# Performance work log

Hardware: AMD Instinct MI355X
Metric: run time of the kernel (lower is better)

The kernel has to match this reference:

```python
import jax, jax.numpy as jnp
import numpy as np

B, N = 2, 8192

PARAM_SHAPES = {
    'down0_w': (32, 3), 'down0_b': (32,),
    'sc1_w1': (32, 35), 'sc1_b1': (32,), 'sc1_w2': (64, 32), 'sc1_b2': (64,),
    'sc2_w1': (64, 67), 'sc2_b1': (64,), 'sc2_w2': (128, 64), 'sc2_b2': (128,),
    'sc3_w1': (128, 131), 'sc3_b1': (128,), 'sc3_w2': (192, 128), 'sc3_b2': (192,),
    'sc4_w1': (192, 195), 'sc4_b1': (192,), 'sc4_w2': (192, 192), 'sc4_b2': (192,),
    'up4_w1': (192, 195), 'up4_b1': (192,), 'up4_w2': (192, 384), 'up4_b2': (192,),
    'up3_w1': (128, 195), 'up3_b1': (128,), 'up3_w2': (128, 256), 'up3_b2': (128,),
    'up2_w1': (64, 131), 'up2_b1': (64,), 'up2_w2': (64, 128), 'up2_b2': (64,),
    'up1_w1': (32, 67), 'up1_b1': (32,), 'up1_w2': (32, 64), 'up1_b2': (32,),
}
PNAMES = list(PARAM_SHAPES.keys())


def _fps(xyz, m):
    # xyz [N,3] -> [m] int32 farthest-point-sample indices (deterministic, start at point 0)
    def body(dmin, _):
        nxt = jnp.argmax(dmin)
        d = jnp.sum((xyz - xyz[nxt]) ** 2, -1)
        return jnp.minimum(dmin, d), nxt.astype(jnp.int32)
    d0 = jnp.sum((xyz - xyz[0]) ** 2, -1)
    _, rest = jax.lax.scan(body, d0, None, length=m - 1)
    return jnp.concatenate([jnp.zeros((1,), jnp.int32), rest])


def _gather(pts, idx):
    # pts [B,N,C], idx [B,...] -> [B,...,C]
    return jax.vmap(lambda p, i: p[i])(pts, idx)


def _ball_query(new_xyz, xyz, radius, k):
    # first-k points within radius, invalid slots filled with the first valid index
    d2 = jnp.sum((new_xyz[:, :, None, :] - xyz[:, None, :, :]) ** 2, -1)  # [B,M,N]
    n = xyz.shape[1]
    order = jnp.where(d2 <= radius * radius, jnp.arange(n)[None, None, :], n)
    idx = jnp.argsort(order, axis=-1)[..., :k]
    valid = jnp.take_along_axis(order, idx, -1) < n
    return jnp.where(valid, idx, idx[..., :1])


def _knn(query, ref, k):
    d2 = jnp.sum((query[:, :, None, :] - ref[:, None, :, :]) ** 2, -1)  # [B,Nq,Nr]
    _, idx = jax.lax.top_k(-d2, k)
    return idx


def _mlp(h, w, b):
    # pointwise shared MLP layer with ReLU on channel-last tensor
    return jax.nn.relu(jnp.einsum('...c,oc->...o', h, w) + b)


def _set_conv(xyz, feat, npoint, radius, k, w1, b1, w2, b2):
    # PointNet++-style SetConv: FPS -> ball-query group -> shared MLP -> max-pool
    fps_idx = jax.vmap(_fps, (0, None))(xyz, npoint)          # [B,M]
    new_xyz = _gather(xyz, fps_idx)                            # [B,M,3]
    gi = _ball_query(new_xyz, xyz, radius, k)                  # [B,M,k]
    h = jnp.concatenate([_gather(xyz, gi) - new_xyz[:, :, None, :], _gather(feat, gi)], -1)
    h = _mlp(_mlp(h, w1, b1), w2, b2)                          # [B,M,k,Cout]
    return new_xyz, fps_idx, jnp.max(h, axis=2)


def _set_upconv(s_xyz, d_xyz, s_feat, d_feat, k, w1, b1, w2, b2):
    # FlowNet3D-style SetUpConv: kNN from dense to sparse -> MLP -> max-pool -> fuse with dense feat
    gi = _knn(d_xyz, s_xyz, k)                                 # [B,Nd,k]
    h = jnp.concatenate([_gather(s_xyz, gi) - d_xyz[:, :, None, :], _gather(s_feat, gi)], -1)
    pooled = jnp.max(_mlp(h, w1, b1), axis=2)                  # [B,Nd,m1]
    return _mlp(jnp.concatenate([pooled, d_feat], -1), w2, b2)


def _encoder(pc, feat, p):
    xyz = jnp.transpose(pc, (0, 2, 1))                         # [B,N,3]
    f0 = _mlp(jnp.transpose(feat, (0, 2, 1)), p['down0_w'], p['down0_b'])  # [B,N,32]
    xyz1, i1, f1 = _set_conv(xyz, f0, 2048, 0.5, 16, p['sc1_w1'], p['sc1_b1'], p['sc1_w2'], p['sc1_b2'])
    xyz2, i2, f2 = _set_conv(xyz1, f1, 512, 1.0, 16, p['sc2_w1'], p['sc2_b1'], p['sc2_w2'], p['sc2_b2'])
    xyz3, i3, f3 = _set_conv(xyz2, f2, 128, 2.0, 16, p['sc3_w1'], p['sc3_b1'], p['sc3_w2'], p['sc3_b2'])
    xyz4, i4, f4 = _set_conv(xyz3, f3, 64, 4.0, 16, p['sc4_w1'], p['sc4_b1'], p['sc4_w2'], p['sc4_b2'])
    u3 = _set_upconv(xyz4, xyz3, f4, f3, 8, p['up4_w1'], p['up4_b1'], p['up4_w2'], p['up4_b2'])
    u2 = _set_upconv(xyz3, xyz2, u3, f2, 8, p['up3_w1'], p['up3_b1'], p['up3_w2'], p['up3_b2'])
    u1 = _set_upconv(xyz2, xyz1, u2, f1, 8, p['up2_w1'], p['up2_b1'], p['up2_w2'], p['up2_b2'])
    u0 = _set_upconv(xyz1, xyz, u1, f0, 8, p['up1_w1'], p['up1_b1'], p['up1_w2'], p['up1_b2'])
    return (xyz1, xyz2, xyz3), (i1, i2, i3), (u0, u1, u2, u3)


def setup_inputs() -> dict:
    key = jax.random.key(0)
    ks = jax.random.split(key, 2 + len(PNAMES))
    inp = {
        'pc': jax.random.normal(ks[0], (B, 3, N), jnp.float32),
        'feat': jax.random.normal(ks[1], (B, 3, N), jnp.float32),
    }
    for i, name in enumerate(PNAMES):
        inp[name] = jax.random.normal(ks[2 + i], PARAM_SHAPES[name], jnp.float32) * 0.05
    return inp


def reference(pc, feat, down0_w, down0_b, sc1_w1, sc1_b1, sc1_w2, sc1_b2, sc2_w1, sc2_b1, sc2_w2, sc2_b2, sc3_w1, sc3_b1, sc3_w2, sc3_b2, sc4_w1, sc4_b1, sc4_w2, sc4_b2, up4_w1, up4_b1, up4_w2, up4_b2, up3_w1, up3_b1, up3_w2, up3_b2, up2_w1, up2_b1, up2_w2, up2_b2, up1_w1, up1_b1, up1_w2, up1_b2):
    # GenFlow_unit.forward with gts[0] is None -> pure encoder path
    loc = locals()
    p = {k: loc[k] for k in PNAMES}
    (x1, x2, x3), (i1, i2, i3), (u0, u1, u2, u3) = _encoder(pc, feat, p)
    t = lambda a: jnp.transpose(a, (0, 2, 1))  # back to torch channel-first convention
    return (t(x1), t(x2), t(x3), i1, i2, i3, t(u0), t(u1), t(u2), t(u3))
```

## Files before the change

### kernel.cpp

```cpp
#include <hip/hip_runtime.h>
#include <hip/hip_bf16.h>
#include <cstdint>

#define DEV __device__ __forceinline__

typedef float f32x2 __attribute__((ext_vector_type(2)));

DEV float sqdist(float ax, float ay, float az, float bx, float by, float bz) {
    float dx = __fsub_rn(ax, bx), dy = __fsub_rn(ay, by), dz = __fsub_rn(az, bz);
    return __fadd_rn(__fadd_rn(__fmul_rn(dx, dx), __fmul_rn(dy, dy)), __fmul_rn(dz, dz));
}

DEV f32x2 sqdist2(f32x2 ax, f32x2 ay, f32x2 az, float bx, float by, float bz) {
#pragma clang fp contract(off)
    f32x2 dx = ax - bx, dy = ay - by, dz = az - bz;
    return (dx * dx + dy * dy) + dz * dz;
}

DEV unsigned short f2bf(float f) {
    unsigned int u = __float_as_uint(f);
    u += 0x7fffu + ((u >> 16) & 1u);
    return (unsigned short)(u >> 16);
}

DEV float bf2f(unsigned short u) { return __uint_as_float(((unsigned int)u) << 16); }

template <int CTRL>
DEV int dpp_i(int v) { return __builtin_amdgcn_update_dpp(v, v, CTRL, 0xf, 0xf, false); }
template <int CTRL>
DEV float dpp_f(float v) { return __int_as_float(dpp_i<CTRL>(__float_as_int(v))); }

enum : int {
    O_X1 = 0, O_X2 = 12288, O_X3 = 15360,
    O_I1 = 16128, O_I2 = 20224, O_I3 = 21248,
    O_U0 = 21504, O_U1 = 545792, O_U2 = 807936, O_U3 = 939008
};

__global__ __launch_bounds__(256) void k_init(const float* __restrict__ pc,
                                              const float* __restrict__ feat,
                                              const float* __restrict__ w0,
                                              const float* __restrict__ b0,
                                              float* __restrict__ xyz,
                                              unsigned short* __restrict__ f0) {
    const int N = 8192;
    int i = blockIdx.x * blockDim.x + threadIdx.x;
    if (i >= 2 * N) return;
    int b = i / N, n = i % N;
    float fx0 = feat[(b * 3 + 0) * N + n];
    float fx1 = feat[(b * 3 + 1) * N + n];
    float fx2 = feat[(b * 3 + 2) * N + n];
    xyz[i * 3 + 0] = pc[(b * 3 + 0) * N + n];
    xyz[i * 3 + 1] = pc[(b * 3 + 1) * N + n];
    xyz[i * 3 + 2] = pc[(b * 3 + 2) * N + n];
#pragma unroll
    for (int o = 0; o < 32; o++) {
        float acc = b0[o];
        acc = fmaf(w0[o * 3 + 0], fx0, acc);
        acc = fmaf(w0[o * 3 + 1], fx1, acc);
        acc = fmaf(w0[o * 3 + 2], fx2, acc);
        f0[(size_t)i * 32 + o] = f2bf(fmaxf(acc, 0.f));
    }
}

template <int N, int T>
__global__ __launch_bounds__(T) void k_bin(const float* __restrict__ xyz,
                                           float* __restrict__ xp, float* __restrict__ yp,
                                           float* __restrict__ zp, int* __restrict__ pid) {
    constexpr int W = T / 64;
    int b = blockIdx.x, t = threadIdx.x;
    const float* X = xyz + (size_t)b * N * 3;
    __shared__ float smn[3][W], smx[3][W];
    __shared__ int hist[512], scan[512], cnt[512];
    float mn[3] = {3e38f, 3e38f, 3e38f}, mx[3] = {-3e38f, -3e38f, -3e38f};
    for (int p = t; p < N; p += T) {
        float v[3] = {X[p * 3], X[p * 3 + 1], X[p * 3 + 2]};
#pragma unroll
        for (int a = 0; a < 3; a++) { mn[a] = fminf(mn[a], v[a]); mx[a] = fmaxf(mx[a], v[a]); }
    }
#pragma unroll
    for (int a = 0; a < 3; a++) {
#pragma unroll
        for (int m = 1; m < 64; m <<= 1) {
            mn[a] = fminf(mn[a], __shfl_xor(mn[a], m, 64));
            mx[a] = fmaxf(mx[a], __shfl_xor(mx[a], m, 64));
        }
    }
    if ((t & 63) == 0) {
#pragma unroll
        for (int a = 0; a < 3; a++) { smn[a][t >> 6] = mn[a]; smx[a][t >> 6] = mx[a]; }
    }
    for (int i = t; i < 512; i += T) { hist[i] = 0; cnt[i] = 0; }
    __syncthreads();
#pragma unroll
    for (int a = 0; a < 3; a++) {
        mn[a] = smn[a][0]; mx[a] = smx[a][0];
#pragma unroll
        for (int w = 1; w < W; w++) { mn[a] = fminf(mn[a], smn[a][w]); mx[a] = fmaxf(mx[a], smx[a][w]); }
    }
    float inv[3];
#pragma unroll
    for (int a = 0; a < 3; a++) inv[a] = 8.0f / fmaxf(mx[a] - mn[a], 1e-9f);
    auto bin_of = [&](float x, float y, float z) {
        int ix = min(7, max(0, (int)((x - mn[0]) * inv[0])));
        int iy = min(7, max(0, (int)((y - mn[1]) * inv[1])));
        int iz = min(7, max(0, (int)((z - mn[2]) * inv[2])));
        return (ix << 6) | (iy << 3) | iz;
    };
    for (int p = t; p < N; p += T) {
        atomicAdd(&hist[bin_of(X[p * 3], X[p * 3 + 1], X[p * 3 + 2])], 1);
    }
    __syncthreads();
    if (t < 512) scan[t] = hist[t];
    __syncthreads();
    for (int s = 1; s < 512; s <<= 1) {
        int v = 0;
        if (t < 512 && t >= s) v = scan[t - s];
        __syncthreads();
        if (t < 512) scan[t] += v;
        __syncthreads();
    }
    for (int p = t; p < N; p += T) {
        float x = X[p * 3], y = X[p * 3 + 1], z = X[p * 3 + 2];
        int bid = bin_of(x, y, z);
        int pos = (scan[bid] - hist[bid]) + atomicAdd(&cnt[bid], 1);
        xp[(size_t)b * N + pos] = x;
        yp[(size_t)b * N + pos] = y;
        zp[(size_t)b * N + pos] = z;
        pid[(size_t)b * N + pos] = p;
    }
}

template <int N, int M, int T>
__global__ __launch_bounds__(T, 1) void k_fps_pruned(
    const float* __restrict__ xp, const float* __restrict__ yp,
    const float* __restrict__ zp, const int* __restrict__ pidg,
    const float* __restrict__ xyz, int* __restrict__ idx_out) {
    constexpr int P = N / T;
    constexpr int P2 = P / 2;
    int b = blockIdx.x, t = threadIdx.x;
    const float* XP = xp + (size_t)b * N;
    const float* YP = yp + (size_t)b * N;
    const float* ZP = zp + (size_t)b * N;
    const int* PIDG = pidg + (size_t)b * N;
    __shared__ float sx[N], sy[N], sz[N];
    __shared__ int spid[N];
    __shared__ unsigned long long skey[3];
    f32x2 px[P2], py[P2], pz[P2], dmin[P2];
    float c0x = xyz[(size_t)b * N * 3 + 0];
    float c0y = xyz[(size_t)b * N * 3 + 1];
    float c0z = xyz[(size_t)b * N * 3 + 2];
    int base = t * P;
    float blx = 3e38f, bly = 3e38f, blz = 3e38f, bhx = -3e38f, bhy = -3e38f, bhz = -3e38f;
#pragma unroll
    for (int i = 0; i < P2; i++) {
        int p0 = base + 2 * i, p1 = p0 + 1;
        px[i] = f32x2{XP[p0], XP[p1]};
        py[i] = f32x2{YP[p0], YP[p1]};
        pz[i] = f32x2{ZP[p0], ZP[p1]};
        sx[p0] = px[i].x; sy[p0] = py[i].x; sz[p0] = pz[i].x;
        sx[p1] = px[i].y; sy[p1] = py[i].y; sz[p1] = pz[i].y;
        spid[p0] = PIDG[p0]; spid[p1] = PIDG[p1];
        blx = fminf(blx, fminf(px[i].x, px[i].y)); bhx = fmaxf(bhx, fmaxf(px[i].x, px[i].y));
        bly = fminf(bly, fminf(py[i].x, py[i].y)); bhy = fmaxf(bhy, fmaxf(py[i].x, py[i].y));
        blz = fminf(blz, fminf(pz[i].x, pz[i].y)); bhz = fmaxf(bhz, fmaxf(pz[i].x, pz[i].y));
        dmin[i] = sqdist2(px[i], py[i], pz[i], c0x, c0y, c0z);
    }
    if (t == 0) {
        idx_out[b * M] = 0;
        skey[0] = 0; skey[1] = 0; skey[2] = 0;
    }
    float bv;
    int bi;
    auto local_argmax = [&]() {
        f32x2 m2[P2];
#pragma unroll
        for (int i = 0; i < P2; i++) m2[i] = dmin[i];
#pragma unroll
        for (int s = P2 / 2; s >= 1; s >>= 1)
#pragma unroll
            for (int i = 0; i < s; i++) m2[i] = __builtin_elementwise_max(m2[i], m2[i + s]);
        bv = fmaxf(m2[0].x, m2[0].y);
        int ii[P];
#pragma unroll
        for (int i = 0; i < P; i++)
            ii[i] = (dmin[i >> 1][i & 1] == bv) ? (base + i) : 0x7fffffff;
#pragma unroll
        for (int s = P / 2; s >= 1; s >>= 1)
#pragma unroll
            for (int i = 0; i < s; i++) ii[i] = min(ii[i], ii[i + s]);
        bi = ii[0];
    };
    float bvw;
    int biw;
    auto wave_reduce = [&]() {
        float bw = bv;
        bw = fmaxf(bw, dpp_f<0x121>(bw));
        bw = fmaxf(bw, dpp_f<0x122>(bw));
        bw = fmaxf(bw, dpp_f<0x124>(bw));
        bw = fmaxf(bw, dpp_f<0x128>(bw));
        bw = fmaxf(bw, dpp_f<0x142>(bw));
        bw = fmaxf(bw, dpp_f<0x143>(bw));
        bvw = __int_as_float(__builtin_amdgcn_readlane(__float_as_int(bw), 63));
        unsigned int im = (bv == bvw) ? (unsigned int)bi : 0xffffffffu;
        im = min(im, (unsigned int)dpp_i<0x121>((int)im));
        im = min(im, (unsigned int)dpp_i<0x122>((int)im));
        im = min(im, (unsigned int)dpp_i<0x124>((int)im));
        im = min(im, (unsigned int)dpp_i<0x128>((int)im));
        im = min(im, (unsigned int)dpp_i<0x142>((int)im));
        im = min(im, (unsigned int)dpp_i<0x143>((int)im));
        biw = __builtin_amdgcn_readlane((int)im, 63);
    };
    local_argmax();
    wave_reduce();
    __syncthreads();
    int jm = 1;
    for (int j = 1; j < M; j++) {
        unsigned long long key =
            ((unsigned long long)__float_as_uint(bvw) << 32) | (unsigned int)~biw;
        if ((t & 63) == 0) atomicMax(&skey[jm], key);
        __syncthreads();
        unsigned long long gk = skey[jm];
        int gi = (int)~(unsigned int)gk;
        if (t == 0) {
            idx_out[b * M + j] = spid[gi];
            skey[jm == 0 ? 2 : jm - 1] = 0;
        }
        jm = (jm == 2) ? 0 : jm + 1;
        float cx = sx[gi], cy = sy[gi], cz = sz[gi];
        float qx = fminf(fmaxf(cx, blx), bhx);
        float qy = fminf(fmaxf(cy, bly), bhy);
        float qz = fminf(fmaxf(cz, blz), bhz);
        float dxb = cx - qx, dyb = cy - qy, dzb = cz - qz;
        float db = dxb * dxb + dyb * dyb + dzb * dzb;
        bool upd = !(db * 0.999f > bv);
        if (upd) {
#pragma unroll
            for (int i = 0; i < P2; i++)
                dmin[i] = __builtin_elementwise_min(
                    dmin[i], sqdist2(px[i], py[i], pz[i], cx, cy, cz));
            local_argmax();
        }
        if (__ballot(upd)) wave_reduce();
    }
}

template <int N, int M, int T>
DEV void fps_body(int b, int t, const float* __restrict__ xyz,
                  int* __restrict__ idx_out, char* smem) {
    constexpr int P = N / T;
    constexpr int P2 = P / 2;
    constexpr int W = T / 64;
    const float* X = xyz + (size_t)b * N * 3;
    float* sx = (float*)smem;
    float* sy = sx + N;
    float* sz = sy + N;
    unsigned long long* skey = (unsigned long long*)(smem + 12 * N);
    f32x2 px[P2], py[P2], pz[P2], dmin[P2];
    float c0x = X[0], c0y = X[1], c0z = X[2];
#pragma unroll
    for (int i = 0; i < P2; i++) {
        int p0 = (2 * i) * T + t, p1 = (2 * i + 1) * T + t;
        px[i] = f32x2{X[p0 * 3 + 0], X[p1 * 3 + 0]};
        py[i] = f32x2{X[p0 * 3 + 1], X[p1 * 3 + 1]};
        pz[i] = f32x2{X[p0 * 3 + 2], X[p1 * 3 + 2]};
        sx[p0] = px[i].x; sy[p0] = py[i].x; sz[p0] = pz[i].x;
        sx[p1] = px[i].y; sy[p1] = py[i].y; sz[p1] = pz[i].y;
        dmin[i] = sqdist2(px[i], py[i], pz[i], c0x, c0y, c0z);
    }
    if (t == 0) {
        idx_out[b * M] = 0;
        skey[0] = 0; skey[1] = 0; skey[2] = 0;
    }
    __syncthreads();
    int jm = 1;
    for (int j = 1; j < M; j++) {
        f32x2 m2[P2];
#pragma unroll
        for (int i = 0; i < P2; i++) m2[i] = dmin[i];
#pragma unroll
        for (int s = P2 / 2; s >= 1; s >>= 1)
#pragma unroll
            for (int i = 0; i < s; i++) m2[i] = __builtin_elementwise_max(m2[i], m2[i + s]);
        float bv = fmaxf(m2[0].x, m2[0].y);
        int ii[P];
#pragma unroll
        for (int i = 0; i < P; i++)
            ii[i] = (dmin[i >> 1][i & 1] == bv) ? (i * T + t) : 0x7fffffff;
#pragma unroll
        for (int s = P / 2; s >= 1; s >>= 1)
#pragma unroll
            for (int i = 0; i < s; i++) ii[i] = min(ii[i], ii[i + s]);
        int bi = ii[0];
        float bw = bv;
        bw = fmaxf(bw, dpp_f<0x121>(bw));
        bw = fmaxf(bw, dpp_f<0x122>(bw));
        bw = fmaxf(bw, dpp_f<0x124>(bw));
        bw = fmaxf(bw, dpp_f<0x128>(bw));
        bw = fmaxf(bw, dpp_f<0x142>(bw));
        bw = fmaxf(bw, dpp_f<0x143>(bw));
        float bvw = __int_as_float(__builtin_amdgcn_readlane(__float_as_int(bw), 63));
        unsigned int im = (bv == bvw) ? (unsigned int)bi : 0xffffffffu;
        im = min(im, (unsigned int)dpp_i<0x121>((int)im));
        im = min(im, (unsigned int)dpp_i<0x122>((int)im));
        im = min(im, (unsigned int)dpp_i<0x124>((int)im));
        im = min(im, (unsigned int)dpp_i<0x128>((int)im));
        im = min(im, (unsigned int)dpp_i<0x142>((int)im));
        im = min(im, (unsigned int)dpp_i<0x143>((int)im));
        int biw = __builtin_amdgcn_readlane((int)im, 63);
        int gi;
        if constexpr (W > 1) {
            unsigned long long key =
                ((unsigned long long)__float_as_uint(bvw) << 32) | (unsigned int)~biw;
            if ((t & 63) == 0) atomicMax(&skey[jm], key);
            __syncthreads();
            unsigned long long gk = skey[jm];
            gi = (int)~(unsigned int)gk;
            if (t == 0) skey[jm == 0 ? 2 : jm - 1] = 0;
            jm = (jm == 2) ? 0 : jm + 1;
        } else {
            gi = biw;
        }
        if (t == 0) idx_out[b * M + j] = gi;
        float cx = sx[gi], cy = sy[gi], cz = sz[gi];
#pragma unroll
        for (int i = 0; i < P2; i++)
            dmin[i] = __builtin_elementwise_min(
                dmin[i], sqdist2(px[i], py[i], pz[i], cx, cy, cz));
    }
}

template <int N, int M, int T>
__global__ __launch_bounds__(T, 1) void k_fps(const float* __restrict__ xyz,
                                              int* __restrict__ idx_out) {
    __shared__ __align__(16) char smem[12 * N + 24];
    fps_body<N, M, T>(blockIdx.x, threadIdx.x, xyz, idx_out, smem);
}

__global__ __launch_bounds__(256) void k_gather(const float* __restrict__ xyz_src,
                                                const int* __restrict__ idx,
                                                float* __restrict__ xyz_dst,
                                                int NS, int M) {
    int i = blockIdx.x * blockDim.x + threadIdx.x;
    if (i >= 2 * M) return;
    int b = i / M;
    int id = idx[i] & (NS - 1);
    xyz_dst[i * 3 + 0] = xyz_src[((size_t)b * NS + id) * 3 + 0];
    xyz_dst[i * 3 + 1] = xyz_src[((size_t)b * NS + id) * 3 + 1];
    xyz_dst[i * 3 + 2] = xyz_src[((size_t)b * NS + id) * 3 + 2];
}

template <int NS, int CF, int CMID, int COUT>
DEV void setconv_body(int q, int bb, int tid, int bdim,
                      const float* __restrict__ X, const unsigned short* __restrict__ F,
                      const float* __restrict__ C, const float* __restrict__ w1,
                      const float* __restrict__ b1, const float* __restrict__ w2,
                      const float* __restrict__ b2, unsigned short* __restrict__ fout,
                      float r2, int M, char* smem) {
    constexpr int CIN = 3 + CF;
    constexpr int K = 16;
    constexpr int M8 = CMID / 8;
    constexpr int O8 = COUT / 8;
    constexpr int MSTR = CMID + 1;
    int blk = bb * M + q;
    const float* Xb = X + (size_t)bb * NS * 3;
    const unsigned short* Fb = F + (size_t)bb * NS * CF;
    int* s_n = (int*)smem;
    int* s_cntp = (int*)(smem + 64);
    float* s_h = (float*)(smem + 80);
    float* s_mid = s_h + K * CIN;
    float* s_pool = s_mid + K * MSTR;
    float cx = C[(size_t)blk * 3 + 0], cy = C[(size_t)blk * 3 + 1], cz = C[(size_t)blk * 3 + 2];
    if (tid < 64) {
        int lane = tid;
        int cnt = 0;
        for (int base = 0; base < NS; base += 64) {
            int p = base + lane;
            float d2 = sqdist(Xb[p * 3], Xb[p * 3 + 1], Xb[p * 3 + 2], cx, cy, cz);
            bool in = (d2 <= r2);
            unsigned long long msk = __ballot(in);
            if (in) {
                int pos = cnt + __popcll(msk & ((1ull << lane) - 1ull));
                if (pos < K) s_n[pos] = p;
            }
            cnt += __popcll(msk);
            if (cnt >= K) break;
        }
        if (lane == 0) *s_cntp = cnt < K ? cnt : K;
    }
    __syncthreads();
    int cnt = *s_cntp;
    if (tid >= cnt && tid < K) s_n[tid] = s_n[0];
    __syncthreads();
    for (int tIdx = tid; tIdx < K * CIN; tIdx += bdim) {
        int n = tIdx / CIN, c = tIdx % CIN;
        int gi = s_n[n];
        float v;
        if (c < 3) v = __fsub_rn(Xb[gi * 3 + c], (c == 0 ? cx : (c == 1 ? cy : cz)));
        else v = bf2f(Fb[(size_t)gi * CF + (c - 3)]);
        s_h[n * CIN + c] = v;
    }
    __syncthreads();
    if (tid < 128) {
        int n = tid >> 3, sub = tid & 7;
#pragma unroll
        for (int j = 0; j < M8; j++) {
            int m = sub * M8 + j;
            float acc = b1[m];
#pragma unroll 4
            for (int c = 0; c < CIN; c++) acc = fmaf(w1[m * CIN + c], s_h[n * CIN + c], acc);
            s_mid[n * MSTR + m] = fmaxf(acc, 0.f);
        }
    }
    __syncthreads();
    if (tid < 128) {
        int n = tid >> 3, sub = tid & 7;
        float vals[O8];
#pragma unroll
        for (int j = 0; j < O8; j++) {
            int o = sub * O8 + j;
            float acc = b2[o];
#pragma unroll 4
            for (int c = 0; c < CMID; c++) acc = fmaf(w2[o * CMID + c], s_mid[n * MSTR + c], acc);
            vals[j] = fmaxf(acc, 0.f);
        }
#pragma unroll
        for (int j = 0; j < O8; j++) {
            vals[j] = fmaxf(vals[j], __shfl_xor(vals[j], 8, 64));
            vals[j] = fmaxf(vals[j], __shfl_xor(vals[j], 16, 64));
            vals[j] = fmaxf(vals[j], __shfl_xor(vals[j], 32, 64));
        }
        int lw = tid & 63, wv = tid >> 6;
        if (lw < 8) {
#pragma unroll
            for (int j = 0; j < O8; j++) s_pool[wv * COUT + lw * O8 + j] = vals[j];
        }
    }
    __syncthreads();
    if (tid < 8) {
#pragma unroll
        for (int j = 0; j < O8; j++) {
            int o = tid * O8 + j;
            fout[(size_t)blk * COUT + o] = f2bf(fmaxf(s_pool[o], s_pool[COUT + o]));
        }
    }
}

template <int NS, int CF, int CMID, int COUT>
__global__ __launch_bounds__(128) void k_setconv(
    const float* __restrict__ X, const unsigned short* __restrict__ F,
    const float* __restrict__ C, const float* __restrict__ w1,
    const float* __restrict__ b1, const float* __restrict__ w2,
    const float* __restrict__ b2, unsigned short* __restrict__ fout,
    float r2, int M) {
    constexpr int K = 16;
    constexpr int CIN = 3 + CF;
    __shared__ __align__(16) char smem[80 + 4 * (K * CIN + K * (CMID + 1) + 2 * COUT)];
    setconv_body<NS, CF, CMID, COUT>(blockIdx.x, blockIdx.y, threadIdx.x, blockDim.x,
                                     X, F, C, w1, b1, w2, b2, fout, r2, M, smem);
}

template <int N, int M, int T, int NS, int CF, int CMID, int COUT>
__global__ __launch_bounds__(T, 1) void k_fps_sc(
    const float* __restrict__ fxyz, int* __restrict__ idx_out,
    const float* __restrict__ X, const unsigned short* __restrict__ F,
    const float* __restrict__ C, const float* __restrict__ w1,
    const float* __restrict__ b1, const float* __restrict__ w2,
    const float* __restrict__ b2, unsigned short* __restrict__ fout,
    float r2, int Msc) {
    constexpr int K = 16;
    constexpr int CIN = 3 + CF;
    constexpr int FPS_B = 12 * N + 24;
    constexpr int SC_B = 80 + 4 * (K * CIN + K * (CMID + 1) + 2 * COUT);
    constexpr int SB = FPS_B > SC_B ? FPS_B : SC_B;
    __shared__ __align__(16) char smem[SB];
    if (blockIdx.x < 2) {
        fps_body<N, M, T>(blockIdx.x, threadIdx.x, fxyz, idx_out, smem);
    } else {
        int lin = blockIdx.x - 2;
        int q = lin % Msc, bb = lin / Msc;
        setconv_body<NS, CF, CMID, COUT>(q, bb, threadIdx.x, blockDim.x,
                                         X, F, C, w1, b1, w2, b2, fout, r2, Msc, smem);
    }
}

template <int S, int CS, int CMID, int CD, int COUT, bool TRANS>
__global__ __launch_bounds__(64) void k_upconv(
    const float* __restrict__ SX, const float* __restrict__ DX,
    const void* __restrict__ SFv, const unsigned short* __restrict__ DF,
    const float* __restrict__ w1, const float* __restrict__ b1,
    const float* __restrict__ w2, const float* __restrict__ b2,
    float* __restrict__ out, int o_off, int ND) {
    constexpr int K = 8;
    constexpr int CIN = 3 + CS;
    constexpr int CIN2 = CMID + CD;
    constexpr int M8 = CMID / 8;
    int q = blockIdx.x, b = blockIdx.y;
    int blk = b * ND + q;
    int lane = threadIdx.x;
    const float* SXb = SX + (size_t)b * S * 3;
    float qx = DX[(size_t)blk * 3], qy = DX[(size_t)blk * 3 + 1], qz = DX[(size_t)blk * 3 + 2];
    __shared__ int s_k[K];
    __shared__ float s_h[K][CIN];
    __shared__ float s_in2[CIN2];
    float bd[K];
    int bi[K];
#pragma unroll
    for (int i = 0; i < K; i++) { bd[i] = 3.0e38f; bi[i] = 0x7fffffff; }
    for (int p = lane; p < S; p += 64) {
        float d2 = sqdist(SXb[p * 3], SXb[p * 3 + 1], SXb[p * 3 + 2], qx, qy, qz);
        if (d2 < bd[K - 1] || (d2 == bd[K - 1] && p < bi[K - 1])) {
            bd[K - 1] = d2; bi[K - 1] = p;
#pragma unroll
            for (int j = K - 1; j > 0; j--) {
                bool sw = (bd[j] < bd[j - 1]) || (bd[j] == bd[j - 1] && bi[j] < bi[j - 1]);
                if (sw) {
                    float tv = bd[j]; bd[j] = bd[j - 1]; bd[j - 1] = tv;
                    int ti = bi[j]; bi[j] = bi[j - 1]; bi[j - 1] = ti;
                }
            }
        }
    }
    for (int r = 0; r < K; r++) {
        float vv = bd[0];
        float bw = vv;
        bw = fminf(bw, dpp_f<0x121>(bw));
        bw = fminf(bw, dpp_f<0x122>(bw));
        bw = fminf(bw, dpp_f<0x124>(bw));
        bw = fminf(bw, dpp_f<0x128>(bw));
        bw = fminf(bw, dpp_f<0x142>(bw));
        bw = fminf(bw, dpp_f<0x143>(bw));
        float vw = __int_as_float(__builtin_amdgcn_readlane(__float_as_int(bw), 63));
        unsigned int im = (vv == vw) ? (unsigned int)bi[0] : 0xffffffffu;
        im = min(im, (unsigned int)dpp_i<0x121>((int)im));
        im = min(im, (unsigned int)dpp_i<0x122>((int)im));
        im = min(im, (unsigned int)dpp_i<0x124>((int)im));
        im = min(im, (unsigned int)dpp_i<0x128>((int)im));
        im = min(im, (unsigned int)dpp_i<0x142>((int)im));
        im = min(im, (unsigned int)dpp_i<0x143>((int)im));
        int iw = __builtin_amdgcn_readlane((int)im, 63);
        if (lane == 0) s_k[r] = iw;
        if (iw == bi[0]) {
#pragma unroll
            for (int j = 0; j < K - 1; j++) { bd[j] = bd[j + 1]; bi[j] = bi[j + 1]; }
            bd[K - 1] = 3.0e38f; bi[K - 1] = 0x7fffffff;
        }
    }
    __syncthreads();
    for (int tIdx = lane; tIdx < K * CIN; tIdx += 64) {
        int n = tIdx / CIN, c = tIdx % CIN;
        int gi = s_k[n];
        float v;
        if (c < 3) v = __fsub_rn(SXb[gi * 3 + c], (c == 0 ? qx : (c == 1 ? qy : qz)));
        else if (TRANS) v = ((const float*)SFv)[((size_t)b * CS + (c - 3)) * S + gi];
        else v = bf2f(((const unsigned short*)SFv)[((size_t)b * S + gi) * CS + (c - 3)]);
        s_h[n][c] = v;
    }
    for (int c = lane; c < CD; c += 64) s_in2[CMID + c] = bf2f(DF[(size_t)blk * CD + c]);
    __syncthreads();
    int n = lane >> 3, sub = lane & 7;
    float vals[M8];
#pragma unroll
    for (int j = 0; j < M8; j++) {
        int m = sub * M8 + j;
        float acc = b1[m];
#pragma unroll 4
        for (int c = 0; c < CIN; c++) acc = fmaf(w1[m * CIN + c], s_h[n][c], acc);
        vals[j] = fmaxf(acc, 0.f);
    }
#pragma unroll
    for (int j = 0; j < M8; j++) {
        vals[j] = fmaxf(vals[j], __shfl_xor(vals[j], 8, 64));
        vals[j] = fmaxf(vals[j], __shfl_xor(vals[j], 16, 64));
        vals[j] = fmaxf(vals[j], __shfl_xor(vals[j], 32, 64));
    }
    if (lane < 8) {
#pragma unroll
        for (int j = 0; j < M8; j++) s_in2[lane * M8 + j] = vals[j];
    }
    __syncthreads();
    for (int o = lane; o < COUT; o += 64) {
        float acc = b2[o];
#pragma unroll 4
        for (int c = 0; c < CIN2; c++) acc = fmaf(w2[o * CIN2 + c], s_in2[c], acc);
        out[o_off + ((size_t)b * COUT + o) * ND + q] = fmaxf(acc, 0.f);
    }
}

__global__ __launch_bounds__(256) void k_finalize(
    const float* __restrict__ xyz1, const float* __restrict__ xyz2,
    const float* __restrict__ xyz3, const int* __restrict__ idx1,
    const int* __restrict__ idx2, const int* __restrict__ idx3,
    float* __restrict__ out) {
    int i = blockIdx.x * blockDim.x + threadIdx.x;
    const float* xs;
    const int* is;
    int M, ox, oi, j;
    if (i < 4096) { xs = xyz1; is = idx1; M = 2048; ox = O_X1; oi = O_I1; j = i; }
    else if (i < 5120) { xs = xyz2; is = idx2; M = 512; ox = O_X2; oi = O_I2; j = i - 4096; }
    else if (i < 5376) { xs = xyz3; is = idx3; M = 128; ox = O_X3; oi = O_I3; j = i - 5120; }
    else return;
    int b = j / M, m = j % M;
    out[ox + (b * 3 + 0) * M + m] = xs[j * 3 + 0];
    out[ox + (b * 3 + 1) * M + m] = xs[j * 3 + 1];
    out[ox + (b * 3 + 2) * M + m] = xs[j * 3 + 2];
    out[oi + j] = (float)is[j];
}

extern "C" void kernel_launch(void* const* d_in, const int* in_sizes, int n_in,
                              void* d_out, int out_size, void* d_ws, size_t ws_size,
                              hipStream_t stream) {
    const float* pc = (const float*)d_in[0];
    const float* feat = (const float*)d_in[1];
    const float* w0 = (const float*)d_in[2];
    const float* b0v = (const float*)d_in[3];
    const float* sc1w1 = (const float*)d_in[4];  const float* sc1b1 = (const float*)d_in[5];
    const float* sc1w2 = (const float*)d_in[6];  const float* sc1b2 = (const float*)d_in[7];
    const float* sc2w1 = (const float*)d_in[8];  const float* sc2b1 = (const float*)d_in[9];
    const float* sc2w2 = (const float*)d_in[10]; const float* sc2b2 = (const float*)d_in[11];
    const float* sc3w1 = (const float*)d_in[12]; const float* sc3b1 = (const float*)d_in[13];
    const float* sc3w2 = (const float*)d_in[14]; const float* sc3b2 = (const float*)d_in[15];
    const float* sc4w1 = (const float*)d_in[16]; const float* sc4b1 = (const float*)d_in[17];
    const float* sc4w2 = (const float*)d_in[18]; const float* sc4b2 = (const float*)d_in[19];
    const float* up4w1 = (const float*)d_in[20]; const float* up4b1 = (const float*)d_in[21];
    const float* up4w2 = (const float*)d_in[22]; const float* up4b2 = (const float*)d_in[23];
    const float* up3w1 = (const float*)d_in[24]; const float* up3b1 = (const float*)d_in[25];
    const float* up3w2 = (const float*)d_in[26]; const float* up3b2 = (const float*)d_in[27];
    const float* up2w1 = (const float*)d_in[28]; const float* up2b1 = (const float*)d_in[29];
    const float* up2w2 = (const float*)d_in[30]; const float* up2b2 = (const float*)d_in[31];
    const float* up1w1 = (const float*)d_in[32]; const float* up1b1 = (const float*)d_in[33];
    const float* up1w2 = (const float*)d_in[34]; const float* up1b2 = (const float*)d_in[35];
    float* out = (float*)d_out;

    char* ws = (char*)d_ws;
    size_t off = 0;
    auto A = [&](size_t bytes) -> char* {
        char* p = ws + off;
        off += (bytes + 255) & ~(size_t)255;
        return p;
    };
    float* xyz  = (float*)A((size_t)2 * 8192 * 3 * 4);
    int* idx1   = (int*)A((size_t)2 * 2048 * 4);
    int* idx2   = (int*)A((size_t)2 * 512 * 4);
    int* idx3   = (int*)A((size_t)2 * 128 * 4);
    int* idx4   = (int*)A((size_t)2 * 64 * 4);
    float* xyz1 = (float*)A((size_t)2 * 2048 * 3 * 4);
    float* xyz2 = (float*)A((size_t)2 * 512 * 3 * 4);
    float* xyz3 = (float*)A((size_t)2 * 128 * 3 * 4);
    float* xyz4 = (float*)A((size_t)2 * 64 * 3 * 4);
    unsigned short* f0 = (unsigned short*)A((size_t)2 * 8192 * 32 * 2);
    unsigned short* f1 = (unsigned short*)A((size_t)2 * 2048 * 64 * 2);
    unsigned short* f2 = (unsigned short*)A((size_t)2 * 512 * 128 * 2);
    unsigned short* f3 = (unsigned short*)A((size_t)2 * 128 * 192 * 2);
    unsigned short* f4 = (unsigned short*)A((size_t)2 * 64 * 192 * 2);
    float* xp  = (float*)A((size_t)2 * 8192 * 4);
    float* yp  = (float*)A((size_t)2 * 8192 * 4);
    float* zp  = (float*)A((size_t)2 * 8192 * 4);
    int* pid   = (int*)A((size_t)2 * 8192 * 4);

    k_init<<<(2 * 8192 + 255) / 256, 256, 0, stream>>>(pc, feat, w0, b0v, xyz, f0);

    k_bin<8192, 512><<<2, 512, 0, stream>>>(xyz, xp, yp, zp, pid);
    k_fps_pruned<8192, 2048, 512><<<2, 512, 0, stream>>>(xp, yp, zp, pid, xyz, idx1);
    k_gather<<<16, 256, 0, stream>>>(xyz, idx1, xyz1, 8192, 2048);
    k_fps_sc<2048, 512, 512, 8192, 32, 32, 64><<<2 + 2 * 2048, 512, 0, stream>>>(
        xyz1, idx2, xyz, f0, xyz1, sc1w1, sc1b1, sc1w2, sc1b2, f1, 0.25f, 2048);
    k_gather<<<4, 256, 0, stream>>>(xyz1, idx2, xyz2, 2048, 512);
    k_fps_sc<512, 128, 256, 2048, 64, 64, 128><<<2 + 2 * 512, 256, 0, stream>>>(
        xyz2, idx3, xyz1, f1, xyz2, sc2w1, sc2b1, sc2w2, sc2b2, f2, 1.0f, 512);
    k_gather<<<1, 256, 0, stream>>>(xyz2, idx3, xyz3, 512, 128);
    k_fps<128, 64, 64><<<2, 64, 0, stream>>>(xyz3, idx4);
    k_gather<<<1, 128, 0, stream>>>(xyz3, idx4, xyz4, 128, 64);
    k_setconv<512, 128, 128, 192><<<dim3(128, 2), 128, 0, stream>>>(
        xyz2, f2, xyz3, sc3w1, sc3b1, sc3w2, sc3b2, f3, 4.0f, 128);
    k_setconv<128, 192, 192, 192><<<dim3(64, 2), 128, 0, stream>>>(
        xyz3, f3, xyz4, sc4w1, sc4b1, sc4w2, sc4b2, f4, 16.0f, 64);

    k_upconv<64, 192, 192, 192, 192, false><<<dim3(128, 2), 64, 0, stream>>>(
        xyz4, xyz3, f4, f3, up4w1, up4b1, up4w2, up4b2, out, O_U3, 128);
    k_upconv<128, 192, 128, 128, 128, true><<<dim3(512, 2), 64, 0, stream>>>(
        xyz3, xyz2, out + O_U3, f2, up3w1, up3b1, up3w2, up3b2, out, O_U2, 512);
    k_upconv<512, 128, 64, 64, 64, true><<<dim3(2048, 2), 64, 0, stream>>>(
        xyz2, xyz1, out + O_U2, f1, up2w1, up2b1, up2w2, up2b2, out, O_U1, 2048);
    k_upconv<2048, 64, 32, 32, 32, true><<<dim3(8192, 2), 64, 0, stream>>>(
        xyz1, xyz, out + O_U1, f0, up1w1, up1b1, up1w2, up1b2, out, O_U0, 8192);

    k_finalize<<<(5376 + 255) / 256, 256, 0, stream>>>(
        xyz1, xyz2, xyz3, idx1, idx2, idx3, out);
}
```

Before: 3.674 ms.

## Use spatially binned pruned FPS for second and third set-conv levels

Applies the bin-sorted, bounding-box-pruned FPS already used at level one to the 2048- and 512-point FPS stages fused into the set-conv kernels. Each level adds a k_bin pass to build spatially sorted coordinate arrays. The plain k_fps is simplified to a single-wave version without shared atomics. The aim is to skip distance updates for threads whose point cluster cannot change, at the cost of an extra binning launch and more shared memory for each FPS block.

```diff
diff --git a/kernel.cpp b/kernel.cpp
--- a/kernel.cpp
+++ b/kernel.cpp
@@ -131,20 +131,22 @@
 }
 
 template <int N, int M, int T>
-__global__ __launch_bounds__(T, 1) void k_fps_pruned(
-    const float* __restrict__ xp, const float* __restrict__ yp,
-    const float* __restrict__ zp, const int* __restrict__ pidg,
-    const float* __restrict__ xyz, int* __restrict__ idx_out) {
+DEV void fps_pruned_body(int b, int t,
+                         const float* __restrict__ xp, const float* __restrict__ yp,
+                         const float* __restrict__ zp, const int* __restrict__ pidg,
+                         const float* __restrict__ xyz, int* __restrict__ idx_out,
+                         char* smem) {
     constexpr int P = N / T;
     constexpr int P2 = P / 2;
-    int b = blockIdx.x, t = threadIdx.x;
     const float* XP = xp + (size_t)b * N;
     const float* YP = yp + (size_t)b * N;
     const float* ZP = zp + (size_t)b * N;
     const int* PIDG = pidg + (size_t)b * N;
-    __shared__ float sx[N], sy[N], sz[N];
-    __shared__ int spid[N];
-    __shared__ unsigned long long skey[3];
+    float* sx = (float*)smem;
+    float* sy = sx + N;
+    float* sz = sy + N;
+    int* spid = (int*)(sz + N);
+    unsigned long long* skey = (unsigned long long*)(smem + 16 * N);
     f32x2 px[P2], py[P2], pz[P2], dmin[P2];
     float c0x = xyz[(size_t)b * N * 3 + 0];
     float c0y = xyz[(size_t)b * N * 3 + 1];
@@ -245,16 +247,23 @@
 }
 
 template <int N, int M, int T>
-DEV void fps_body(int b, int t, const float* __restrict__ xyz,
-                  int* __restrict__ idx_out, char* smem) {
+__global__ __launch_bounds__(T, 1) void k_fps_pruned(
+    const float* __restrict__ xp, const float* __restrict__ yp,
+    const float* __restrict__ zp, const int* __restrict__ pidg,
+    const float* __restrict__ xyz, int* __restrict__ idx_out) {
+    __shared__ __align__(16) char smem[16 * N + 24];
+    fps_pruned_body<N, M, T>(blockIdx.x, threadIdx.x, xp, yp, zp, pidg, xyz,
+                             idx_out, smem);
+}
+
+template <int N, int M, int T>
+__global__ __launch_bounds__(T, 1) void k_fps(const float* __restrict__ xyz,
+                                              int* __restrict__ idx_out) {
     constexpr int P = N / T;
     constexpr int P2 = P / 2;
-    constexpr int W = T / 64;
+    int b = blockIdx.x, t = threadIdx.x;
     const float* X = xyz + (size_t)b * N * 3;
-    float* sx = (float*)smem;
-    float* sy = sx + N;
-    float* sz = sy + N;
-    unsigned long long* skey = (unsigned long long*)(smem + 12 * N);
+    __shared__ float sx[N], sy[N], sz[N];
     f32x2 px[P2], py[P2], pz[P2], dmin[P2];
     float c0x = X[0], c0y = X[1], c0z = X[2];
 #pragma unroll
@@ -267,12 +276,8 @@
         sx[p1] = px[i].y; sy[p1] = py[i].y; sz[p1] = pz[i].y;
         dmin[i] = sqdist2(px[i], py[i], pz[i], c0x, c0y, c0z);
     }
-    if (t == 0) {
-        idx_out[b * M] = 0;
-        skey[0] = 0; skey[1] = 0; skey[2] = 0;
-    }
-    __syncthreads();
-    int jm = 1;
+    if (t == 0) idx_out[b * M] = 0;
+    __builtin_amdgcn_s_waitcnt(0);
     for (int j = 1; j < M; j++) {
         f32x2 m2[P2];
 #pragma unroll
@@ -306,20 +311,7 @@
         im = min(im, (unsigned int)dpp_i<0x128>((int)im));
         im = min(im, (unsigned int)dpp_i<0x142>((int)im));
         im = min(im, (unsigned int)dpp_i<0x143>((int)im));
-        int biw = __builtin_amdgcn_readlane((int)im, 63);
-        int gi;
-        if constexpr (W > 1) {
-            unsigned long long key =
-                ((unsigned long long)__float_as_uint(bvw) << 32) | (unsigned int)~biw;
-            if ((t & 63) == 0) atomicMax(&skey[jm], key);
-            __syncthreads();
-            unsigned long long gk = skey[jm];
-            gi = (int)~(unsigned int)gk;
-            if (t == 0) skey[jm == 0 ? 2 : jm - 1] = 0;
-            jm = (jm == 2) ? 0 : jm + 1;
-        } else {
-            gi = biw;
-        }
+        int gi = __builtin_amdgcn_readlane((int)im, 63);
         if (t == 0) idx_out[b * M + j] = gi;
         float cx = sx[gi], cy = sy[gi], cz = sz[gi];
 #pragma unroll
@@ -327,13 +319,6 @@
             dmin[i] = __builtin_elementwise_min(
                 dmin[i], sqdist2(px[i], py[i], pz[i], cx, cy, cz));
     }
-}
-
-template <int N, int M, int T>
-__global__ __launch_bounds__(T, 1) void k_fps(const float* __restrict__ xyz,
-                                              int* __restrict__ idx_out) {
-    __shared__ __align__(16) char smem[12 * N + 24];
-    fps_body<N, M, T>(blockIdx.x, threadIdx.x, xyz, idx_out, smem);
 }
 
 __global__ __launch_bounds__(256) void k_gather(const float* __restrict__ xyz_src,
@@ -460,7 +445,9 @@
 }
 
 template <int N, int M, int T, int NS, int CF, int CMID, int COUT>
-__global__ __launch_bounds__(T, 1) void k_fps_sc(
+__global__ __launch_bounds__(T, 1) void k_fps_psc(
+    const float* __restrict__ fxp, const float* __restrict__ fyp,
+    const float* __restrict__ fzp, const int* __restrict__ fpid,
     const float* __restrict__ fxyz, int* __restrict__ idx_out,
     const float* __restrict__ X, const unsigned short* __restrict__ F,
     const float* __restrict__ C, const float* __restrict__ w1,
@@ -469,12 +456,13 @@
     float r2, int Msc) {
     constexpr int K = 16;
     constexpr int CIN = 3 + CF;
-    constexpr int FPS_B = 12 * N + 24;
+    constexpr int FPS_B = 16 * N + 24;
     constexpr int SC_B = 80 + 4 * (K * CIN + K * (CMID + 1) + 2 * COUT);
     constexpr int SB = FPS_B > SC_B ? FPS_B : SC_B;
     __shared__ __align__(16) char smem[SB];
     if (blockIdx.x < 2) {
-        fps_body<N, M, T>(blockIdx.x, threadIdx.x, fxyz, idx_out, smem);
+        fps_pruned_body<N, M, T>(blockIdx.x, threadIdx.x, fxp, fyp, fzp, fpid,
+                                 fxyz, idx_out, smem);
     } else {
         int lin = blockIdx.x - 2;
         int q = lin % Msc, bb = lin / Msc;
@@ -656,17 +644,29 @@
     float* yp  = (float*)A((size_t)2 * 8192 * 4);
     float* zp  = (float*)A((size_t)2 * 8192 * 4);
     int* pid   = (int*)A((size_t)2 * 8192 * 4);
+    float* xp2 = (float*)A((size_t)2 * 2048 * 4);
+    float* yp2 = (float*)A((size_t)2 * 2048 * 4);
+    float* zp2 = (float*)A((size_t)2 * 2048 * 4);
+    int* pid2  = (int*)A((size_t)2 * 2048 * 4);
+    float* xp3 = (float*)A((size_t)2 * 512 * 4);
+    float* yp3 = (float*)A((size_t)2 * 512 * 4);
+    float* zp3 = (float*)A((size_t)2 * 512 * 4);
+    int* pid3  = (int*)A((size_t)2 * 512 * 4);
 
     k_init<<<(2 * 8192 + 255) / 256, 256, 0, stream>>>(pc, feat, w0, b0v, xyz, f0);
 
     k_bin<8192, 512><<<2, 512, 0, stream>>>(xyz, xp, yp, zp, pid);
     k_fps_pruned<8192, 2048, 512><<<2, 512, 0, stream>>>(xp, yp, zp, pid, xyz, idx1);
     k_gather<<<16, 256, 0, stream>>>(xyz, idx1, xyz1, 8192, 2048);
-    k_fps_sc<2048, 512, 512, 8192, 32, 32, 64><<<2 + 2 * 2048, 512, 0, stream>>>(
-        xyz1, idx2, xyz, f0, xyz1, sc1w1, sc1b1, sc1w2, sc1b2, f1, 0.25f, 2048);
+    k_bin<2048, 512><<<2, 512, 0, stream>>>(xyz1, xp2, yp2, zp2, pid2);
+    k_fps_psc<2048, 512, 512, 8192, 32, 32, 64><<<2 + 2 * 2048, 512, 0, stream>>>(
+        xp2, yp2, zp2, pid2, xyz1, idx2,
+        xyz, f0, xyz1, sc1w1, sc1b1, sc1w2, sc1b2, f1, 0.25f, 2048);
     k_gather<<<4, 256, 0, stream>>>(xyz1, idx2, xyz2, 2048, 512);
-    k_fps_sc<512, 128, 256, 2048, 64, 64, 128><<<2 + 2 * 512, 256, 0, stream>>>(
-        xyz2, idx3, xyz1, f1, xyz2, sc2w1, sc2b1, sc2w2, sc2b2, f2, 1.0f, 512);
+    k_bin<512, 512><<<2, 512, 0, stream>>>(xyz2, xp3, yp3, zp3, pid3);
+    k_fps_psc<512, 128, 256, 2048, 64, 64, 128><<<2 + 2 * 512, 256, 0, stream>>>(
+        xp3, yp3, zp3, pid3, xyz2, idx3,
+        xyz1, f1, xyz2, sc2w1, sc2b1, sc2w2, sc2b2, f2, 1.0f, 512);
     k_gather<<<1, 256, 0, stream>>>(xyz2, idx3, xyz3, 512, 128);
     k_fps<128, 64, 64><<<2, 64, 0, stream>>>(xyz3, idx4);
     k_gather<<<1, 128, 0, stream>>>(xyz3, idx4, xyz4, 128, 64);
```

New measurement: 3.666 ms. Within noise of the previous version (-0.2%).
